# Kernel optimization log

Measured on AMD Instinct MI355X. Metric: run time of the kernel, lower is better.

Reference implementation:

```python
import jax, jax.numpy as jnp
import numpy as np

N = 131072
D = 1024
L = 128
B = 64  # number of bags / segments
TEMP = 1.0
EPS = 1e-12  # F.normalize eps


def setup_inputs() -> dict:
    key = jax.random.key(0)
    ks = jax.random.split(key, 5)
    feature = jax.random.normal(ks[0], (N, D), dtype=jnp.float32)
    batch = jnp.sort(jax.random.randint(ks[1], (N,), 0, B)).astype(jnp.int64)
    # xavier_normal_ std = sqrt(2 / (fan_in + fan_out))
    Wa = jax.random.normal(ks[2], (L, D), dtype=jnp.float32) * np.sqrt(2.0 / (D + L))
    Wb = jax.random.normal(ks[3], (L, D), dtype=jnp.float32) * np.sqrt(2.0 / (D + L))
    Wc = jax.random.normal(ks[4], (1, L), dtype=jnp.float32) * np.sqrt(2.0 / (L + 1))
    ba = jnp.zeros((L,), dtype=jnp.float32)
    bb = jnp.zeros((L,), dtype=jnp.float32)
    bc = jnp.zeros((1,), dtype=jnp.float32)
    return {"feature": feature, "batch": batch, "Wa": Wa, "ba": ba,
            "Wb": Wb, "bb": bb, "Wc": Wc, "bc": bc}


def reference(feature, batch, Wa, ba, Wb, bb, Wc, bc):
    # F.normalize: L2-normalize each row
    norm = jnp.linalg.norm(feature, axis=1, keepdims=True)
    feature = feature / jnp.maximum(norm, EPS)

    # gated attention score
    a = jax.nn.sigmoid(feature @ Wa.T + ba)            # [N, L]
    b = jnp.tanh(feature @ Wb.T + bb)                  # [N, L]
    score = ((a * b) @ Wc.T + bc) / TEMP               # [N, 1]

    # segment softmax over bags (torch_geometric softmax(score, batch))
    s = score[:, 0]                                    # [N]
    seg_max = jax.ops.segment_max(s, batch, num_segments=B)
    e = jnp.exp(s - seg_max[batch])
    denom = jax.ops.segment_sum(e, batch, num_segments=B)
    score = (e / denom[batch])[:, None]                # [N, 1]

    # scatter-sum pooling (dropout omitted: eval-mode determinism)
    out = jax.ops.segment_sum(score * feature, batch, num_segments=B)  # [B, D]
    return (out, score, feature)
```

## Files before the change

### kernel.cpp

```cpp
#include <hip/hip_runtime.h>
#include <hip/hip_bf16.h>
#include <cstdint>
#include <cstddef>

#define NROWS 131072
#define DDIM  1024
#define LDIM  128
#define BSEG  64
#define FIX2  281474976710656.0

typedef float f32x4 __attribute__((ext_vector_type(4)));
typedef short short8 __attribute__((ext_vector_type(8)));

__device__ inline unsigned short f2bf(float f) {
    union { float f; unsigned u; } x; x.f = f;
    unsigned u = x.u + 0x7fffu + ((x.u >> 16) & 1u);
    return (unsigned short)(u >> 16);
}

__device__ inline int lower_bound_dev(const int* __restrict__ arr, int n, int v) {
    int lo = 0, hi = n;
    while (lo < hi) { int mid = (lo + hi) >> 1; if (arr[mid] < v) lo = mid + 1; else hi = mid; }
    return lo;
}

__global__ void wconv_kernel(const float* __restrict__ Wa, const float* __restrict__ Wb,
                             unsigned short* __restrict__ wpre) {
    int n  = blockIdx.x;
    int kt = threadIdx.x >> 4;
    int q  = threadIdx.x & 15;
    const float* wrow = (n < LDIM) ? (Wa + (size_t)n * DDIM)
                                   : (Wb + (size_t)(n - LDIM) * DDIM);
    float4 v = *(const float4*)(wrow + kt * 64 + q * 4);
    ushort4 h;
    h.x = f2bf(v.x); h.y = f2bf(v.y); h.z = f2bf(v.z); h.w = f2bf(v.w);
    int w, nfi, rA;
    if (n < LDIM) { w = n >> 4; nfi = 0; rA = n & 15; }
    else { int m = n - LDIM; w = m >> 4; nfi = 1; rA = m & 15; }
    int kk    = q >> 3;
    int e     = (q & 7) * 4;
    int kl    = e >> 3;
    int inner = (e & 7) * 2;
    int lane  = kl * 16 + rA;
    int f     = ((kt * 2 + kk) * 8 + w) * 2 + nfi;
    *(ushort4*)((char*)wpre + f * 1024 + lane * 16 + inner) = h;
}

__global__ __launch_bounds__(512, 6)
void gemm_kernel(const float* __restrict__ feat, const unsigned short* __restrict__ wpre,
                 const float* __restrict__ ba, const float* __restrict__ bb,
                 const float* __restrict__ Wc, const float* __restrict__ bc,
                 const int* __restrict__ batch,
                 float* __restrict__ nf_out, float* __restrict__ s_out,
                 unsigned long long* __restrict__ acc64)
{
    __shared__ __align__(16) char smem[35584];
    float* invA_l = (float*)(smem + 32768);
    float* part   = (float*)(smem + 33024);
    float* u_row  = (float*)(smem + 35072);
    int*   seg_l  = (int*)(smem + 35328);

    const int tid  = threadIdx.x;
    const int w    = tid >> 6;
    const int lane = tid & 63;
    const int rblk = blockIdx.x * 64;
    const int sr   = tid >> 3;
    const int sc8  = tid & 7;

    if (tid < 64) seg_l[tid] = batch[rblk + tid];

    const float4* rowp4 = (const float4*)(feat + (size_t)(rblk + sr) * DDIM);

    f32x4 acc[4][2];
    #pragma unroll
    for (int i = 0; i < 4; ++i)
        #pragma unroll
        for (int j = 0; j < 2; ++j)
            acc[i][j] = (f32x4){0.f, 0.f, 0.f, 0.f};

    const int rA  = lane & 15;
    const int kl  = lane >> 4;
    const int swz = (lane & 7) << 4;
    const char* wsrc = (const char*)wpre + w * 2048 + lane * 16;

    float4 av1_0, av1_1, av2_0, av2_1;
    float sq = 0.f;

    #pragma unroll
    for (int j = 0; j < 2; ++j) {
        int cf = sc8 + j * 8;
        float4 v = rowp4[cf];
        sq += v.x * v.x + v.y * v.y + v.z * v.z + v.w * v.w;
        union { ushort4 h; __hip_bfloat162 b2[2]; } cv;
        cv.b2[0] = __float22bfloat162_rn(make_float2(v.x, v.y));
        cv.b2[1] = __float22bfloat162_rn(make_float2(v.z, v.w));
        *(ushort4*)(smem + ((sr * 128 + cf * 8) ^ ((sr & 7) << 4))) = cv.h;
    }
    av1_0 = rowp4[16 + sc8];
    av1_1 = rowp4[16 + sc8 + 8];
    __syncthreads();

    int cur = 0;
    for (int kt = 0; kt < 16; ++kt) {
        short8 wf[4];
        #pragma unroll
        for (int q = 0; q < 4; ++q)
            wf[q] = *(const short8*)(wsrc + (size_t)kt * 32768 + (q >> 1) * 16384 + (q & 1) * 1024);
        if (kt < 14) {
            av2_0 = rowp4[(kt + 2) * 16 + sc8];
            av2_1 = rowp4[(kt + 2) * 16 + sc8 + 8];
        }
        {
            const char* Abuf = smem + cur * 16384;
            #pragma unroll
            for (int kk = 0; kk < 2; ++kk) {
                int koff = (kk * 64 + kl * 16) ^ swz;
                #pragma unroll
                for (int mf = 0; mf < 4; ++mf) {
                    short8 af = *(const short8*)(Abuf + (mf * 16 + rA) * 128 + koff);
                    #pragma unroll
                    for (int nfi = 0; nfi < 2; ++nfi)
                        acc[mf][nfi] = __builtin_amdgcn_mfma_f32_16x16x32_bf16(
                            af, wf[kk * 2 + nfi], acc[mf][nfi], 0, 0, 0);
                }
            }
        }
        if (kt < 15) {
            char* Ab2 = smem + (cur ^ 1) * 16384;
            #pragma unroll
            for (int j = 0; j < 2; ++j) {
                int cf = sc8 + j * 8;
                float4 v = (j == 0) ? av1_0 : av1_1;
                sq += v.x * v.x + v.y * v.y + v.z * v.z + v.w * v.w;
                union { ushort4 h; __hip_bfloat162 b2[2]; } cv;
                cv.b2[0] = __float22bfloat162_rn(make_float2(v.x, v.y));
                cv.b2[1] = __float22bfloat162_rn(make_float2(v.z, v.w));
                *(ushort4*)(Ab2 + ((sr * 128 + cf * 8) ^ ((sr & 7) << 4))) = cv.h;
            }
        }
        asm volatile("s_waitcnt lgkmcnt(0)\n\ts_barrier" ::: "memory");
        cur ^= 1;
        av1_0 = av2_0; av1_1 = av2_1;
    }

    sq += __shfl_xor(sq, 1, 64);
    sq += __shfl_xor(sq, 2, 64);
    sq += __shfl_xor(sq, 4, 64);
    if (sc8 == 0) invA_l[sr] = 1.f / fmaxf(sqrtf(sq), 1e-12f);
    __syncthreads();

    {
        int l0 = w * 16 + rA;
        float ba0 = ba[l0], bb0 = bb[l0], wc0 = Wc[l0];
        float vals[4][4];
        #pragma unroll
        for (int mf = 0; mf < 4; ++mf)
            #pragma unroll
            for (int reg = 0; reg < 4; ++reg) {
                int r = mf * 16 + kl * 4 + reg;
                float ia = invA_l[r];
                float pa0 = acc[mf][0][reg] * ia + ba0;
                float pb0 = acc[mf][1][reg] * ia + bb0;
                float a0 = 1.f / (1.f + __expf(-pa0));
                float b0 = 1.f - 2.f / (1.f + __expf(2.f * pb0));
                vals[mf][reg] = a0 * b0 * wc0;
            }
        #pragma unroll
        for (int mf = 0; mf < 4; ++mf)
            #pragma unroll
            for (int reg = 0; reg < 4; ++reg) {
                float v = vals[mf][reg];
                v += __shfl_xor(v, 1, 64);
                v += __shfl_xor(v, 2, 64);
                v += __shfl_xor(v, 4, 64);
                v += __shfl_xor(v, 8, 64);
                vals[mf][reg] = v;
            }
        if (rA == 0) {
            #pragma unroll
            for (int mf = 0; mf < 4; ++mf)
                #pragma unroll
                for (int reg = 0; reg < 4; ++reg)
                    part[w * 64 + mf * 16 + kl * 4 + reg] = vals[mf][reg];
        }
    }
    __syncthreads();
    if (tid < 64) {
        float s = part[tid] + part[64 + tid] + part[128 + tid] + part[192 + tid]
                + part[256 + tid] + part[320 + tid] + part[384 + tid] + part[448 + tid] + bc[0];
        u_row[tid] = __expf(s);
        s_out[rblk + tid] = s;
    }
    __syncthreads();

    {
        const int col = tid & 255;
        const int grp = tid >> 8;
        const float4* __restrict__ fbase = (const float4*)(feat + (size_t)rblk * DDIM);
        float4*       __restrict__ nbase = (float4*)(nf_out + (size_t)rblk * DDIM);
        float ax = 0.f, ay = 0.f, az = 0.f, aw = 0.f;
        int curseg = seg_l[grp];
        for (int rr = 0; rr < 8; ++rr) {
            int r0 = rr * 8 + grp;
            float4 v0 = fbase[(r0 + 0) * 256 + col];
            float4 v1 = fbase[(r0 + 2) * 256 + col];
            float4 v2 = fbase[(r0 + 4) * 256 + col];
            float4 v3 = fbase[(r0 + 6) * 256 + col];
            #pragma unroll
            for (int j = 0; j < 4; ++j) {
                int r = r0 + j * 2;
                float4 v = (j == 0) ? v0 : (j == 1) ? v1 : (j == 2) ? v2 : v3;
                int sg = seg_l[r];
                if (sg != curseg) {
                    unsigned long long* dst = acc64 + (size_t)curseg * DDIM + col * 4;
                    atomicAdd(&dst[0], (unsigned long long)(long long)((double)ax * FIX2));
                    atomicAdd(&dst[1], (unsigned long long)(long long)((double)ay * FIX2));
                    atomicAdd(&dst[2], (unsigned long long)(long long)((double)az * FIX2));
                    atomicAdd(&dst[3], (unsigned long long)(long long)((double)aw * FIX2));
                    ax = ay = az = aw = 0.f;
                    curseg = sg;
                }
                float ia = invA_l[r];
                float u  = u_row[r];
                v.x *= ia; v.y *= ia; v.z *= ia; v.w *= ia;
                nbase[r * 256 + col] = v;
                ax += u * v.x; ay += u * v.y; az += u * v.z; aw += u * v.w;
            }
        }
        unsigned long long* dst = acc64 + (size_t)curseg * DDIM + col * 4;
        atomicAdd(&dst[0], (unsigned long long)(long long)((double)ax * FIX2));
        atomicAdd(&dst[1], (unsigned long long)(long long)((double)ay * FIX2));
        atomicAdd(&dst[2], (unsigned long long)(long long)((double)az * FIX2));
        atomicAdd(&dst[3], (unsigned long long)(long long)((double)aw * FIX2));
    }
}

__global__ void softmax_kernel(const int* __restrict__ batch, float* __restrict__ score,
                               float* __restrict__ smax, float* __restrict__ ssum) {
    int b = blockIdx.x;
    int tid = threadIdx.x;
    int start = lower_bound_dev(batch, NROWS, b);
    int end   = lower_bound_dev(batch, NROWS, b + 1);
    __shared__ float red[4];
    __shared__ float bm, bd;

    float m = -INFINITY;
    for (int i = start + tid; i < end; i += 256) m = fmaxf(m, score[i]);
    #pragma unroll
    for (int k = 1; k < 64; k <<= 1) m = fmaxf(m, __shfl_xor(m, k, 64));
    if ((tid & 63) == 0) red[tid >> 6] = m;
    __syncthreads();
    if (tid == 0) bm = fmaxf(fmaxf(red[0], red[1]), fmaxf(red[2], red[3]));
    __syncthreads();
    float M = bm;

    float sum = 0.f;
    for (int i = start + tid; i < end; i += 256) sum += __expf(score[i] - M);
    #pragma unroll
    for (int k = 1; k < 64; k <<= 1) sum += __shfl_xor(sum, k, 64);
    if ((tid & 63) == 0) red[tid >> 6] = sum;
    __syncthreads();
    if (tid == 0) { bd = red[0] + red[1] + red[2] + red[3]; smax[b] = bm; ssum[b] = bd; }
    __syncthreads();
    float invD = 1.f / bd;

    for (int i = start + tid; i < end; i += 256)
        score[i] = __expf(score[i] - M) * invD;
}

__global__ void finalize_kernel(const unsigned long long* __restrict__ acc64,
                                const float* __restrict__ smax, const float* __restrict__ ssum,
                                float* __restrict__ out) {
    int i = blockIdx.x * 256 + threadIdx.x;
    int b = i >> 10;
    double denom = exp((double)smax[b]) * (double)ssum[b];
    out[i] = (float)(((double)(long long)acc64[i]) * (1.0 / FIX2) / denom);
}

extern "C" void kernel_launch(void* const* d_in, const int* in_sizes, int n_in,
                              void* d_out, int out_size, void* d_ws, size_t ws_size,
                              hipStream_t stream) {
    const float* feat  = (const float*)d_in[0];
    const int*   batch = (const int*)d_in[1];
    const float* Wa = (const float*)d_in[2];
    const float* ba = (const float*)d_in[3];
    const float* Wb = (const float*)d_in[4];
    const float* bb = (const float*)d_in[5];
    const float* Wc = (const float*)d_in[6];
    const float* bc = (const float*)d_in[7];

    float* out_seg = (float*)d_out;
    float* score   = out_seg + (size_t)BSEG * DDIM;
    float* nf      = score + NROWS;

    unsigned short*     wpre  = (unsigned short*)d_ws;
    unsigned long long* acc64 = (unsigned long long*)((char*)d_ws + 524288);
    float* smax = (float*)d_ws;
    float* ssum = smax + BSEG;

    hipMemsetAsync(acc64, 0, (size_t)BSEG * DDIM * 8, stream);
    wconv_kernel<<<256, 256, 0, stream>>>(Wa, Wb, wpre);
    gemm_kernel<<<NROWS / 64, 512, 0, stream>>>(feat, wpre, ba, bb, Wc, bc, batch,
                                                nf, score, acc64);
    softmax_kernel<<<BSEG, 256, 0, stream>>>(batch, score, smax, ssum);
    finalize_kernel<<<BSEG * DDIM / 256, 256, 0, stream>>>(acc64, smax, ssum, out_seg);
}
```

Before: 383.4 us.

## Stage whole 32-row bf16 tile in LDS and drop per-k double-buffered pipeline

Halves the row tile from 64 to 32 rows per block and loads the entire bf16-converted row block (all 1024 columns) into LDS in one pass up front, computing the L2 norm before the GEMM instead of interleaving it. The k-loop then runs with no barriers, reading A fragments straight from the resident tile. This removes the per-k-step synchronisation and double buffering, but raises LDS use to about 66KB and lowers occupancy, and the weights are re-read from cache by twice as many blocks.

New measurement: 401.1 us. +4.6%, slower.

```diff
diff --git a/kernel.cpp b/kernel.cpp
--- a/kernel.cpp
+++ b/kernel.cpp
@@ -7,6 +7,7 @@
 #define DDIM  1024
 #define LDIM  128
 #define BSEG  64
+#define BM    32
 #define FIX2  281474976710656.0
 
 typedef float f32x4 __attribute__((ext_vector_type(4)));
@@ -46,7 +47,7 @@
     *(ushort4*)((char*)wpre + f * 1024 + lane * 16 + inner) = h;
 }
 
-__global__ __launch_bounds__(512, 6)
+__global__ __launch_bounds__(512, 4)
 void gemm_kernel(const float* __restrict__ feat, const unsigned short* __restrict__ wpre,
                  const float* __restrict__ ba, const float* __restrict__ bb,
                  const float* __restrict__ Wc, const float* __restrict__ bc,
@@ -54,107 +55,89 @@
                  float* __restrict__ nf_out, float* __restrict__ s_out,
                  unsigned long long* __restrict__ acc64)
 {
-    __shared__ __align__(16) char smem[35584];
-    float* invA_l = (float*)(smem + 32768);
-    float* part   = (float*)(smem + 33024);
-    float* u_row  = (float*)(smem + 35072);
-    int*   seg_l  = (int*)(smem + 35328);
+    __shared__ __align__(16) char smem[66944];
+    float* invA_l = (float*)(smem + 65536);
+    float* part   = (float*)(smem + 65664);
+    float* u_row  = (float*)(smem + 66688);
+    int*   seg_l  = (int*)(smem + 66816);
 
     const int tid  = threadIdx.x;
     const int w    = tid >> 6;
     const int lane = tid & 63;
-    const int rblk = blockIdx.x * 64;
-    const int sr   = tid >> 3;
-    const int sc8  = tid & 7;
-
-    if (tid < 64) seg_l[tid] = batch[rblk + tid];
-
-    const float4* rowp4 = (const float4*)(feat + (size_t)(rblk + sr) * DDIM);
-
-    f32x4 acc[4][2];
-    #pragma unroll
-    for (int i = 0; i < 4; ++i)
-        #pragma unroll
-        for (int j = 0; j < 2; ++j)
-            acc[i][j] = (f32x4){0.f, 0.f, 0.f, 0.f};
-
-    const int rA  = lane & 15;
-    const int kl  = lane >> 4;
-    const int swz = (lane & 7) << 4;
-    const char* wsrc = (const char*)wpre + w * 2048 + lane * 16;
-
-    float4 av1_0, av1_1, av2_0, av2_1;
-    float sq = 0.f;
-
-    #pragma unroll
-    for (int j = 0; j < 2; ++j) {
-        int cf = sc8 + j * 8;
-        float4 v = rowp4[cf];
-        sq += v.x * v.x + v.y * v.y + v.z * v.z + v.w * v.w;
-        union { ushort4 h; __hip_bfloat162 b2[2]; } cv;
-        cv.b2[0] = __float22bfloat162_rn(make_float2(v.x, v.y));
-        cv.b2[1] = __float22bfloat162_rn(make_float2(v.z, v.w));
-        *(ushort4*)(smem + ((sr * 128 + cf * 8) ^ ((sr & 7) << 4))) = cv.h;
-    }
-    av1_0 = rowp4[16 + sc8];
-    av1_1 = rowp4[16 + sc8 + 8];
-    __syncthreads();
-
-    int cur = 0;
-    for (int kt = 0; kt < 16; ++kt) {
-        short8 wf[4];
-        #pragma unroll
-        for (int q = 0; q < 4; ++q)
-            wf[q] = *(const short8*)(wsrc + (size_t)kt * 32768 + (q >> 1) * 16384 + (q & 1) * 1024);
-        if (kt < 14) {
-            av2_0 = rowp4[(kt + 2) * 16 + sc8];
-            av2_1 = rowp4[(kt + 2) * 16 + sc8 + 8];
-        }
-        {
-            const char* Abuf = smem + cur * 16384;
-            #pragma unroll
-            for (int kk = 0; kk < 2; ++kk) {
-                int koff = (kk * 64 + kl * 16) ^ swz;
-                #pragma unroll
-                for (int mf = 0; mf < 4; ++mf) {
-                    short8 af = *(const short8*)(Abuf + (mf * 16 + rA) * 128 + koff);
-                    #pragma unroll
-                    for (int nfi = 0; nfi < 2; ++nfi)
-                        acc[mf][nfi] = __builtin_amdgcn_mfma_f32_16x16x32_bf16(
-                            af, wf[kk * 2 + nfi], acc[mf][nfi], 0, 0, 0);
-                }
-            }
-        }
-        if (kt < 15) {
-            char* Ab2 = smem + (cur ^ 1) * 16384;
-            #pragma unroll
-            for (int j = 0; j < 2; ++j) {
-                int cf = sc8 + j * 8;
-                float4 v = (j == 0) ? av1_0 : av1_1;
+    const int rblk = blockIdx.x * BM;
+    const int srow = tid >> 4;
+    const int c16  = tid & 15;
+
+    if (tid < BM) seg_l[tid] = batch[rblk + tid];
+
+    {
+        const float4* rowp4 = (const float4*)(feat + (size_t)(rblk + srow) * DDIM);
+        char* arow = smem + srow * 2048;
+        const int rsw = (srow & 7) << 4;
+        float sq = 0.f;
+        #pragma unroll
+        for (int jc = 0; jc < 2; ++jc) {
+            float4 t[8];
+            #pragma unroll
+            for (int j = 0; j < 8; ++j)
+                t[j] = rowp4[c16 + (jc * 8 + j) * 16];
+            #pragma unroll
+            for (int j = 0; j < 8; ++j) {
+                float4 v = t[j];
                 sq += v.x * v.x + v.y * v.y + v.z * v.z + v.w * v.w;
                 union { ushort4 h; __hip_bfloat162 b2[2]; } cv;
                 cv.b2[0] = __float22bfloat162_rn(make_float2(v.x, v.y));
                 cv.b2[1] = __float22bfloat162_rn(make_float2(v.z, v.w));
-                *(ushort4*)(Ab2 + ((sr * 128 + cf * 8) ^ ((sr & 7) << 4))) = cv.h;
-            }
-        }
-        asm volatile("s_waitcnt lgkmcnt(0)\n\ts_barrier" ::: "memory");
-        cur ^= 1;
-        av1_0 = av2_0; av1_1 = av2_1;
-    }
-
-    sq += __shfl_xor(sq, 1, 64);
-    sq += __shfl_xor(sq, 2, 64);
-    sq += __shfl_xor(sq, 4, 64);
-    if (sc8 == 0) invA_l[sr] = 1.f / fmaxf(sqrtf(sq), 1e-12f);
-    __syncthreads();
+                int f = c16 + (jc * 8 + j) * 16;
+                *(ushort4*)(arow + ((f * 8) ^ rsw)) = cv.h;
+            }
+        }
+        sq += __shfl_xor(sq, 1, 64);
+        sq += __shfl_xor(sq, 2, 64);
+        sq += __shfl_xor(sq, 4, 64);
+        sq += __shfl_xor(sq, 8, 64);
+        if ((lane & 15) == 0) invA_l[srow] = 1.f / fmaxf(sqrtf(sq), 1e-12f);
+    }
+    __syncthreads();
+
+    const int rA = lane & 15;
+    const int kl = lane >> 4;
+    const char* wsrc = (const char*)wpre + w * 2048 + lane * 16;
+
+    f32x4 acc[2][2];
+    #pragma unroll
+    for (int i = 0; i < 2; ++i)
+        #pragma unroll
+        for (int j = 0; j < 2; ++j)
+            acc[i][j] = (f32x4){0.f, 0.f, 0.f, 0.f};
+
+    #pragma unroll
+    for (int kt = 0; kt < 16; ++kt) {
+        short8 wf[4];
+        #pragma unroll
+        for (int q = 0; q < 4; ++q)
+            wf[q] = *(const short8*)(wsrc + (size_t)kt * 32768 + (q >> 1) * 16384 + (q & 1) * 1024);
+        #pragma unroll
+        for (int kk = 0; kk < 2; ++kk) {
+            #pragma unroll
+            for (int mf = 0; mf < 2; ++mf) {
+                int row = mf * 16 + rA;
+                short8 af = *(const short8*)(smem + row * 2048 +
+                                ((kt * 128 + kk * 64 + kl * 16) ^ ((row & 7) << 4)));
+                #pragma unroll
+                for (int nfi = 0; nfi < 2; ++nfi)
+                    acc[mf][nfi] = __builtin_amdgcn_mfma_f32_16x16x32_bf16(
+                        af, wf[kk * 2 + nfi], acc[mf][nfi], 0, 0, 0);
+            }
+        }
+    }
 
     {
         int l0 = w * 16 + rA;
         float ba0 = ba[l0], bb0 = bb[l0], wc0 = Wc[l0];
-        float vals[4][4];
-        #pragma unroll
-        for (int mf = 0; mf < 4; ++mf)
+        float vals[2][4];
+        #pragma unroll
+        for (int mf = 0; mf < 2; ++mf)
             #pragma unroll
             for (int reg = 0; reg < 4; ++reg) {
                 int r = mf * 16 + kl * 4 + reg;
@@ -166,7 +149,7 @@
                 vals[mf][reg] = a0 * b0 * wc0;
             }
         #pragma unroll
-        for (int mf = 0; mf < 4; ++mf)
+        for (int mf = 0; mf < 2; ++mf)
             #pragma unroll
             for (int reg = 0; reg < 4; ++reg) {
                 float v = vals[mf][reg];
@@ -178,16 +161,16 @@
             }
         if (rA == 0) {
             #pragma unroll
-            for (int mf = 0; mf < 4; ++mf)
+            for (int mf = 0; mf < 2; ++mf)
                 #pragma unroll
                 for (int reg = 0; reg < 4; ++reg)
-                    part[w * 64 + mf * 16 + kl * 4 + reg] = vals[mf][reg];
-        }
-    }
-    __syncthreads();
-    if (tid < 64) {
-        float s = part[tid] + part[64 + tid] + part[128 + tid] + part[192 + tid]
-                + part[256 + tid] + part[320 + tid] + part[384 + tid] + part[448 + tid] + bc[0];
+                    part[w * 32 + mf * 16 + kl * 4 + reg] = vals[mf][reg];
+        }
+    }
+    __syncthreads();
+    if (tid < BM) {
+        float s = part[tid] + part[32 + tid] + part[64 + tid] + part[96 + tid]
+                + part[128 + tid] + part[160 + tid] + part[192 + tid] + part[224 + tid] + bc[0];
         u_row[tid] = __expf(s);
         s_out[rblk + tid] = s;
     }
@@ -200,32 +183,25 @@
         float4*       __restrict__ nbase = (float4*)(nf_out + (size_t)rblk * DDIM);
         float ax = 0.f, ay = 0.f, az = 0.f, aw = 0.f;
         int curseg = seg_l[grp];
-        for (int rr = 0; rr < 8; ++rr) {
-            int r0 = rr * 8 + grp;
-            float4 v0 = fbase[(r0 + 0) * 256 + col];
-            float4 v1 = fbase[(r0 + 2) * 256 + col];
-            float4 v2 = fbase[(r0 + 4) * 256 + col];
-            float4 v3 = fbase[(r0 + 6) * 256 + col];
-            #pragma unroll
-            for (int j = 0; j < 4; ++j) {
-                int r = r0 + j * 2;
-                float4 v = (j == 0) ? v0 : (j == 1) ? v1 : (j == 2) ? v2 : v3;
-                int sg = seg_l[r];
-                if (sg != curseg) {
-                    unsigned long long* dst = acc64 + (size_t)curseg * DDIM + col * 4;
-                    atomicAdd(&dst[0], (unsigned long long)(long long)((double)ax * FIX2));
-                    atomicAdd(&dst[1], (unsigned long long)(long long)((double)ay * FIX2));
-                    atomicAdd(&dst[2], (unsigned long long)(long long)((double)az * FIX2));
-                    atomicAdd(&dst[3], (unsigned long long)(long long)((double)aw * FIX2));
-                    ax = ay = az = aw = 0.f;
-                    curseg = sg;
-                }
-                float ia = invA_l[r];
-                float u  = u_row[r];
-                v.x *= ia; v.y *= ia; v.z *= ia; v.w *= ia;
-                nbase[r * 256 + col] = v;
-                ax += u * v.x; ay += u * v.y; az += u * v.z; aw += u * v.w;
-            }
+        #pragma unroll 4
+        for (int rr = 0; rr < 16; ++rr) {
+            int r = rr * 2 + grp;
+            float4 v = fbase[r * 256 + col];
+            int sg = seg_l[r];
+            if (sg != curseg) {
+                unsigned long long* dst = acc64 + (size_t)curseg * DDIM + col * 4;
+                atomicAdd(&dst[0], (unsigned long long)(long long)((double)ax * FIX2));
+                atomicAdd(&dst[1], (unsigned long long)(long long)((double)ay * FIX2));
+                atomicAdd(&dst[2], (unsigned long long)(long long)((double)az * FIX2));
+                atomicAdd(&dst[3], (unsigned long long)(long long)((double)aw * FIX2));
+                ax = ay = az = aw = 0.f;
+                curseg = sg;
+            }
+            float ia = invA_l[r];
+            float u  = u_row[r];
+            v.x *= ia; v.y *= ia; v.z *= ia; v.w *= ia;
+            nbase[r * 256 + col] = v;
+            ax += u * v.x; ay += u * v.y; az += u * v.z; aw += u * v.w;
         }
         unsigned long long* dst = acc64 + (size_t)curseg * DDIM + col * 4;
         atomicAdd(&dst[0], (unsigned long long)(long long)((double)ax * FIX2));
@@ -300,7 +276,7 @@
 
     hipMemsetAsync(acc64, 0, (size_t)BSEG * DDIM * 8, stream);
     wconv_kernel<<<256, 256, 0, stream>>>(Wa, Wb, wpre);
-    gemm_kernel<<<NROWS / 64, 512, 0, stream>>>(feat, wpre, ba, bb, Wc, bc, batch,
+    gemm_kernel<<<NROWS / BM, 512, 0, stream>>>(feat, wpre, ba, bb, Wc, bc, batch,
                                                 nf, score, acc64);
     softmax_kernel<<<BSEG, 256, 0, stream>>>(batch, score, smax, ssum);
     finalize_kernel<<<BSEG * DDIM / 256, 256, 0, stream>>>(acc64, smax, ssum, out_seg);
```
